# Optimization experiments

Hardware: AMD Instinct MI355X
Metric: run time of the kernel (lower is better)

The kernel has to match this reference:

```python
import jax, jax.numpy as jnp
import numpy as np

EPS = 1e-5
GRID_SIZE = 5
SPLINE_ORDER = 3
WINDOW = 16  # local_window_size hardcoded in Block


def _make_grid(in_features):
    h = 2.0 / GRID_SIZE  # grid_range [-1, 1]
    g = (np.arange(-SPLINE_ORDER, GRID_SIZE + SPLINE_ORDER + 1) * h - 1.0).astype(np.float32)
    return jnp.asarray(np.tile(g[None, :], (in_features, 1)))  # (in, 12)


def layer_norm(x, g, b):
    mu = jnp.mean(x, axis=-1, keepdims=True)
    var = jnp.var(x, axis=-1, keepdims=True)
    return (x - mu) * jax.lax.rsqrt(var + EPS) * g + b


def b_splines(x, grid):
    # x: (M, in) -> (M, in, GRID_SIZE + SPLINE_ORDER)
    xe = x[..., None]
    bases = ((xe >= grid[:, :-1]) & (xe < grid[:, 1:])).astype(x.dtype)
    for k in range(1, SPLINE_ORDER + 1):
        bases = ((xe - grid[:, : -(k + 1)]) / (grid[:, k:-1] - grid[:, : -(k + 1)]) * bases[..., :-1]
                 + (grid[:, k + 1:] - xe) / (grid[:, k + 1:] - grid[:, 1:-k]) * bases[..., 1:])
    return bases


def kan_linear(x, base_w, spline_w, spline_scaler, grid):
    base = jax.nn.silu(x) @ base_w.T  # (M, out)
    sw = spline_w * spline_scaler[..., None]  # (out, in, K)
    spline = jnp.einsum('mik,oik->mo', b_splines(x, grid), sw)
    return base + spline


def conv1d(h, w, b):
    # h: (B, C, T), w: (O, I, 3) or (O, I, k); padding 'same' for k=3 pad=1
    pad = (w.shape[-1] - 1) // 2
    out = jax.lax.conv_general_dilated(h, w, window_strides=(1,), padding=[(pad, pad)],
                                       dimension_numbers=('NCH', 'OIH', 'NCH'))
    return out + b[None, :, None]


def setup_inputs() -> dict:
    key = jax.random.key(0)
    ks = jax.random.split(key, 20)
    B, N, C = 8, 1024, 48
    H = 8
    hid = 24
    K = GRID_SIZE + SPLINE_ORDER
    s = 0.05
    inp = {
        'x': jax.random.normal(ks[0], (B, N, C), dtype=jnp.float32),
        'g1': jnp.ones((C,), jnp.float32), 'b1': jnp.zeros((C,), jnp.float32),
        'w_qkv': jax.random.normal(ks[1], (3 * C, C), jnp.float32) * s,
        'w_proj': jax.random.normal(ks[2], (C, C), jnp.float32) * s,
        'b_proj': jnp.zeros((C,), jnp.float32),
        'g2': jnp.ones((C,), jnp.float32), 'b2': jnp.zeros((C,), jnp.float32),
        'bw1': jax.random.normal(ks[3], (hid, C), jnp.float32) * s,
        'sw1': jax.random.normal(ks[4], (hid, C, K), jnp.float32) * s,
        'ss1': jnp.ones((hid, C), jnp.float32),
        'bw2': jax.random.normal(ks[5], (C, hid), jnp.float32) * s,
        'sw2': jax.random.normal(ks[6], (C, hid, K), jnp.float32) * s,
        'ss2': jnp.ones((C, hid), jnp.float32),
        'conv1_w': jax.random.normal(ks[7], (128, C, 3), jnp.float32) * s,
        'conv1_b': jnp.zeros((128,), jnp.float32),
        'conv3_w': jax.random.normal(ks[8], (C, 128, 3), jnp.float32) * s,
        'conv3_b': jnp.zeros((C,), jnp.float32),
        'sc': jnp.asarray(0.1, jnp.float32),
    }
    return inp


def reference(x, g1, b1, w_qkv, w_proj, b_proj, g2, b2,
              bw1, sw1, ss1, bw2, sw2, ss2,
              conv1_w, conv1_b, conv3_w, conv3_b, sc):
    B, N, C = x.shape
    H = 8
    hd = C // H
    scale = hd ** -0.5

    n1 = layer_norm(x, g1, b1)
    qkv = (n1 @ w_qkv.T).reshape(B, N, 3, H, hd)
    q, k, v = (qkv[:, :, 0].transpose(0, 2, 1, 3),
               qkv[:, :, 1].transpose(0, 2, 1, 3),
               qkv[:, :, 2].transpose(0, 2, 1, 3))  # (B, H, N, hd)

    # global attention
    attn_global = jax.nn.softmax(jnp.einsum('bhqd,bhkd->bhqk', q, k) * scale, axis=-1)
    x_global = jnp.einsum('bhqk,bhkd->bhqd', attn_global, v)
    x_global = x_global.transpose(0, 2, 1, 3).reshape(B, N, C)

    # local (non-overlapping window) attention, vectorized over windows
    W = WINDOW
    nw = N // W
    qw = q.reshape(B, H, nw, W, hd)
    kw = k.reshape(B, H, nw, W, hd)
    vw = v.reshape(B, H, nw, W, hd)
    attn_local = jax.nn.softmax(jnp.einsum('bhnqd,bhnkd->bhnqk', qw, kw) * scale, axis=-1)
    x_local = jnp.einsum('bhnqk,bhnkd->bhnqd', attn_local, vw)
    x_local = x_local.reshape(B, H, N, hd).transpose(0, 2, 1, 3).reshape(B, N, C)

    attn_out = (x_global + x_local) @ w_proj.T + b_proj
    x1 = x + attn_out

    # KAN MLP on norm2(x1), flattened tokens
    n2 = layer_norm(x1, g2, b2).reshape(-1, C)
    grid1 = _make_grid(C)
    grid2 = _make_grid(bw1.shape[0])
    kan_h = kan_linear(n2, bw1, sw1, ss1, grid1)
    kan_o = kan_linear(kan_h, bw2, sw2, ss2, grid2).reshape(B, N, C)
    x2 = x1 + kan_o

    # conv residual path on the original input
    h = x.transpose(0, 2, 1)  # (B, C, N)
    h = conv1d(h, conv1_w, conv1_b)
    h = conv1d(h, conv3_w, conv3_b)
    h = h.transpose(0, 2, 1)  # (B, N, C)
    h = layer_norm(h, g1, b1)  # Block reuses norm1 here

    out = sc * h + x2
    return (out, attn_global)
```

## Files before the change

### kernel.cpp

```cpp
#include <hip/hip_runtime.h>

static constexpr int B = 8, N = 1024, C = 48, H = 8, HD = 6, NT = B * N;
static constexpr int QKVO = 3 * C;
static constexpr int HID = 24, KB = 8;
static constexpr int C1 = 128;

#define DEVFN __device__ __forceinline__

DEVFN float wsum(float v) {
#pragma unroll
  for (int m = 32; m; m >>= 1) v += __shfl_xor(v, m, 64);
  return v;
}
DEVFN float wmax(float v) {
#pragma unroll
  for (int m = 32; m; m >>= 1) v = fmaxf(v, __shfl_xor(v, m, 64));
  return v;
}
DEVFN float gsum16(float v) {
#pragma unroll
  for (int m = 8; m; m >>= 1) v += __shfl_xor(v, m, 16);
  return v;
}
DEVFN float gmax16(float v) {
#pragma unroll
  for (int m = 8; m; m >>= 1) v = fmaxf(v, __shfl_xor(v, m, 16));
  return v;
}

DEVFN void bspline8(float x, float* bs) {
  float b[11];
#pragma unroll
  for (int j = 0; j < 11; ++j) {
    float gj = -2.2f + 0.4f * j;
    float gj1 = -2.2f + 0.4f * (j + 1);
    b[j] = (x >= gj && x < gj1) ? 1.0f : 0.0f;
  }
#pragma unroll
  for (int j = 0; j < 10; ++j) {
    float gj = -2.2f + 0.4f * j;
    b[j] = (x - gj) * 2.5f * b[j] + ((gj + 0.8f) - x) * 2.5f * b[j + 1];
  }
#pragma unroll
  for (int j = 0; j < 9; ++j) {
    float gj = -2.2f + 0.4f * j;
    b[j] = (x - gj) * 1.25f * b[j] + ((gj + 1.2f) - x) * 1.25f * b[j + 1];
  }
#pragma unroll
  for (int j = 0; j < 8; ++j) {
    float gj = -2.2f + 0.4f * j;
    bs[j] = (x - gj) * (1.0f / 1.2f) * b[j] + ((gj + 1.6f) - x) * (1.0f / 1.2f) * b[j + 1];
  }
}

__global__ __launch_bounds__(256) void k_ln_qkv(
    const float* __restrict__ x, const float* __restrict__ g1, const float* __restrict__ b1,
    const float* __restrict__ wqkv, float* __restrict__ q, float* __restrict__ k,
    float* __restrict__ v) {
  __shared__ float wl[QKVO * 49];
  __shared__ float nb[4][C];
  int tid = threadIdx.x;
  for (int e = tid; e < QKVO * C; e += 256) wl[(e / C) * 49 + (e % C)] = wqkv[e];
  int wave = tid >> 6, lane = tid & 63;
  int tok = blockIdx.x * 4 + wave;
  const float* xr = x + tok * C;
  float xv = (lane < C) ? xr[lane] : 0.f;
  float s = wsum(xv), s2 = wsum(xv * xv);
  float mean = s * (1.f / C);
  float var = s2 * (1.f / C) - mean * mean;
  float rstd = rsqrtf(var + 1e-5f);
  if (lane < C) nb[wave][lane] = (xv - mean) * rstd * g1[lane] + b1[lane];
  __syncthreads();
  int b = tok >> 10, n = tok & 1023;
#pragma unroll
  for (int r = 0; r < 3; ++r) {
    int o = lane + (r << 6);
    if (o < QKVO) {
      float acc = 0.f;
#pragma unroll
      for (int i = 0; i < C; ++i) acc += nb[wave][i] * wl[o * 49 + i];
      int ssel = o / C;
      int rem = o - ssel * C;
      int hh = rem / HD;
      int d = rem - hh * HD;
      float* dst = ssel == 0 ? q : (ssel == 1 ? k : v);
      dst[((b * H + hh) * N + n) * HD + d] = acc;
    }
  }
}

__global__ __launch_bounds__(256) void k_gattn(
    const float* __restrict__ q, const float* __restrict__ k, const float* __restrict__ v,
    float* __restrict__ attn, float* __restrict__ xg) {
  __shared__ float2 kt[3][N];
  __shared__ float2 vt[3][N];
  int tid = threadIdx.x;
  int bh = blockIdx.x >> 5;
  int rb = blockIdx.x & 31;
  const float* kg = k + bh * N * HD;
  const float* vg = v + bh * N * HD;
  float* ktf = (float*)kt;
  float* vtf = (float*)vt;
  for (int e = tid; e < N * HD; e += 256) {
    int kp = e / 6, d = e - kp * 6;
    int a = (d >> 1) * 2048 + (kp << 1) + (d & 1);
    ktf[a] = kg[e];
    vtf[a] = vg[e];
  }
  __syncthreads();
  int wave = tid >> 6, lane = tid & 63;
  const float scl = 0.40824829046386301637f;
  int b = bh >> 3, hh = bh & 7;
#pragma unroll 1
  for (int rr = 0; rr < 8; ++rr) {
    int qrow = (rb << 5) + (wave << 3) + rr;
    const float2* qp = (const float2*)(q + (bh * N + qrow) * HD);
    float2 q0 = qp[0], q1 = qp[1], q2 = qp[2];
    float sv[16];
    float mx = -1e30f;
#pragma unroll
    for (int it = 0; it < 16; ++it) {
      int kp = lane + (it << 6);
      float2 a0 = kt[0][kp], a1 = kt[1][kp], a2 = kt[2][kp];
      float dp = q0.x * a0.x + q0.y * a0.y + q1.x * a1.x + q1.y * a1.y + q2.x * a2.x + q2.y * a2.y;
      sv[it] = dp * scl;
      mx = fmaxf(mx, sv[it]);
    }
    mx = wmax(mx);
    float sum = 0.f;
#pragma unroll
    for (int it = 0; it < 16; ++it) {
      sv[it] = __expf(sv[it] - mx);
      sum += sv[it];
    }
    sum = wsum(sum);
    float inv = 1.f / sum;
    float a0 = 0, a1 = 0, a2 = 0, a3 = 0, a4 = 0, a5 = 0;
    float* arow = attn + (size_t)(bh * N + qrow) * N;
#pragma unroll
    for (int it = 0; it < 16; ++it) {
      int kp = lane + (it << 6);
      float p = sv[it];
      arow[kp] = p * inv;
      float2 v0 = vt[0][kp], v1 = vt[1][kp], v2 = vt[2][kp];
      a0 += p * v0.x; a1 += p * v0.y; a2 += p * v1.x;
      a3 += p * v1.y; a4 += p * v2.x; a5 += p * v2.y;
    }
    a0 = wsum(a0) * inv; a1 = wsum(a1) * inv; a2 = wsum(a2) * inv;
    a3 = wsum(a3) * inv; a4 = wsum(a4) * inv; a5 = wsum(a5) * inv;
    if (lane == 0) {
      float* o = xg + (b * N + qrow) * C + hh * HD;
      o[0] = a0; o[1] = a1; o[2] = a2; o[3] = a3; o[4] = a4; o[5] = a5;
    }
  }
}

__global__ __launch_bounds__(256) void k_lattn(
    const float* __restrict__ q, const float* __restrict__ k, const float* __restrict__ v,
    float* __restrict__ xl) {
  int tid = threadIdx.x;
  int wave = tid >> 6, lane = tid & 63;
  int win = blockIdx.x * 4 + wave;
  int bh = win >> 6;
  int wloc = win & 63;
  int n0 = wloc << 4;
  int b = bh >> 3, hh = bh & 7;
  int kk = lane & 15, g = lane >> 4;
  const float* kb = k + (bh * N + n0) * HD;
  const float* vb = v + (bh * N + n0) * HD;
  float kv[6], vv[6];
#pragma unroll
  for (int d = 0; d < 6; ++d) {
    kv[d] = kb[kk * 6 + d];
    vv[d] = vb[kk * 6 + d];
  }
  const float scl = 0.40824829046386301637f;
#pragma unroll
  for (int pass = 0; pass < 4; ++pass) {
    int qr = (pass << 2) + g;
    const float* qp = q + (bh * N + n0 + qr) * HD;
    float s = 0.f;
#pragma unroll
    for (int d = 0; d < 6; ++d) s += qp[d] * kv[d];
    s *= scl;
    float mx = gmax16(s);
    float p = __expf(s - mx);
    float sum = gsum16(p);
    float inv = 1.f / sum;
    float o[6];
#pragma unroll
    for (int d = 0; d < 6; ++d) o[d] = gsum16(p * vv[d]) * inv;
    if (kk == 0) {
      float* dst = xl + (size_t)(b * N + n0 + qr) * C + hh * HD;
#pragma unroll
      for (int d = 0; d < 6; ++d) dst[d] = o[d];
    }
  }
}

__global__ __launch_bounds__(256) void k_proj(
    const float* __restrict__ x, const float* __restrict__ xg, const float* __restrict__ xl,
    const float* __restrict__ wp, const float* __restrict__ bp,
    const float* __restrict__ g2, const float* __restrict__ b2,
    float* __restrict__ x1, float* __restrict__ n2) {
  __shared__ float wl[C * 49];
  __shared__ float ab[4][C];
  int tid = threadIdx.x;
  for (int e = tid; e < C * C; e += 256) wl[(e / C) * 49 + (e % C)] = wp[e];
  int wave = tid >> 6, lane = tid & 63;
  int tok = blockIdx.x * 4 + wave;
  if (lane < C) ab[wave][lane] = xg[tok * C + lane] + xl[tok * C + lane];
  __syncthreads();
  float x1v = 0.f;
  if (lane < C) {
    float acc = bp[lane];
#pragma unroll
    for (int i = 0; i < C; ++i) acc += ab[wave][i] * wl[lane * 49 + i];
    x1v = x[tok * C + lane] + acc;
  }
  float s = wsum(lane < C ? x1v : 0.f);
  float s2 = wsum(lane < C ? x1v * x1v : 0.f);
  float mean = s * (1.f / C), var = s2 * (1.f / C) - mean * mean;
  float rstd = rsqrtf(var + 1e-5f);
  if (lane < C) {
    x1[tok * C + lane] = x1v;
    n2[tok * C + lane] = (x1v - mean) * rstd * g2[lane] + b2[lane];
  }
}

__global__ __launch_bounds__(256) void k_kan1(
    const float* __restrict__ n2, const float* __restrict__ bw1,
    const float* __restrict__ sw1, const float* __restrict__ ss1,
    float* __restrict__ kanh) {
  __shared__ float swt[C * KB * HID];
  __shared__ float bwt[C * HID];
  __shared__ float sst[C * HID];
  __shared__ float bas[4][C][KB];
  __shared__ float sil[4][C];
  int tid = threadIdx.x;
  for (int e = tid; e < C * KB * HID; e += 256) {
    int o = e / (C * KB);
    int rem = e - o * (C * KB);
    swt[rem * HID + o] = sw1[e];
  }
  for (int e = tid; e < C * HID; e += 256) {
    int o = e / C, i = e - o * C;
    bwt[i * HID + o] = bw1[e];
    sst[i * HID + o] = ss1[e];
  }
  int wave = tid >> 6, lane = tid & 63;
  int tok = blockIdx.x * 4 + wave;
  if (lane < C) {
    float xv = n2[tok * C + lane];
    sil[wave][lane] = xv / (1.f + __expf(-xv));
    float bs[KB];
    bspline8(xv, bs);
#pragma unroll
    for (int kk = 0; kk < KB; ++kk) bas[wave][lane][kk] = bs[kk];
  }
  __syncthreads();
  int o = lane & 31;
  int hf = lane >> 5;
  float acc = 0.f;
  if (o < HID) {
    int i0 = hf * 24;
#pragma unroll
    for (int ii = 0; ii < 24; ++ii) {
      int i = i0 + ii;
      float sp = 0.f;
#pragma unroll
      for (int kk = 0; kk < KB; ++kk) sp += bas[wave][i][kk] * swt[(i * KB + kk) * HID + o];
      acc += sil[wave][i] * bwt[i * HID + o] + sst[i * HID + o] * sp;
    }
  }
  acc += __shfl_xor(acc, 32, 64);
  if (lane < HID) kanh[tok * HID + lane] = acc;
}

__global__ __launch_bounds__(256) void k_kan2(
    const float* __restrict__ kanh, const float* __restrict__ x1,
    const float* __restrict__ bw2, const float* __restrict__ sw2,
    const float* __restrict__ ss2, float* __restrict__ x2) {
  __shared__ float swt[HID * KB * C];
  __shared__ float bwt[HID * C];
  __shared__ float sst[HID * C];
  __shared__ float bas[4][HID][KB];
  __shared__ float sil[4][HID];
  int tid = threadIdx.x;
  for (int e = tid; e < HID * KB * C; e += 256) {
    int o = e / (HID * KB);
    int rem = e - o * (HID * KB);
    swt[rem * C + o] = sw2[e];
  }
  for (int e = tid; e < HID * C; e += 256) {
    int o = e / HID, i = e - o * HID;
    bwt[i * C + o] = bw2[e];
    sst[i * C + o] = ss2[e];
  }
  int wave = tid >> 6, lane = tid & 63;
  int tok = blockIdx.x * 4 + wave;
  if (lane < HID) {
    float xv = kanh[tok * HID + lane];
    sil[wave][lane] = xv / (1.f + __expf(-xv));
    float bs[KB];
    bspline8(xv, bs);
#pragma unroll
    for (int kk = 0; kk < KB; ++kk) bas[wave][lane][kk] = bs[kk];
  }
  __syncthreads();
  if (lane < C) {
    float acc = 0.f;
#pragma unroll
    for (int i = 0; i < HID; ++i) {
      float sp = 0.f;
#pragma unroll
      for (int kk = 0; kk < KB; ++kk) sp += bas[wave][i][kk] * swt[(i * KB + kk) * C + lane];
      acc += sil[wave][i] * bwt[i * C + lane] + sst[i * C + lane] * sp;
    }
    x2[tok * C + lane] = x1[tok * C + lane] + acc;
  }
}

__global__ __launch_bounds__(256) void k_conv1(
    const float* __restrict__ x, const float* __restrict__ w1, const float* __restrict__ bc1,
    float* __restrict__ h1) {
  __shared__ float wt[72 * C1];
  __shared__ float xr[18 * C];
  int tid = threadIdx.x;
  int b = blockIdx.x >> 6;
  int t0 = (blockIdx.x & 63) << 4;
  for (int e = tid; e < 18 * C; e += 256) {
    int r = e / C, c = e - r * C;
    int n = t0 - 1 + r;
    xr[e] = (n >= 0 && n < N) ? x[(b * N + n) * C + c] : 0.f;
  }
  int wave = tid >> 6, lane = tid & 63;
  float acc0[4] = {0, 0, 0, 0}, acc1[4] = {0, 0, 0, 0};
  for (int hf = 0; hf < 2; ++hf) {
    __syncthreads();
    for (int e = tid; e < 72 * C1; e += 256) {
      int i3 = e / C1, o = e - i3 * C1;
      int ii = i3 / 3, dk = i3 - ii * 3;
      wt[e] = w1[(o * C + hf * 24 + ii) * 3 + dk];
    }
    __syncthreads();
#pragma unroll
    for (int tt = 0; tt < 4; ++tt) {
      int t = (wave << 2) + tt;
      float a0 = acc0[tt], a1 = acc1[tt];
#pragma unroll 8
      for (int ii = 0; ii < 24; ++ii) {
#pragma unroll
        for (int dk = 0; dk < 3; ++dk) {
          float xin = xr[(t + dk) * C + hf * 24 + ii];
          a0 += xin * wt[(ii * 3 + dk) * C1 + lane];
          a1 += xin * wt[(ii * 3 + dk) * C1 + 64 + lane];
        }
      }
      acc0[tt] = a0;
      acc1[tt] = a1;
    }
  }
  float bb0 = bc1[lane], bb1 = bc1[64 + lane];
#pragma unroll
  for (int tt = 0; tt < 4; ++tt) {
    int n = t0 + (wave << 2) + tt;
    h1[(b * N + n) * C1 + lane] = acc0[tt] + bb0;
    h1[(b * N + n) * C1 + 64 + lane] = acc1[tt] + bb1;
  }
}

__global__ __launch_bounds__(256) void k_conv2out(
    const float* __restrict__ h1, const float* __restrict__ w3, const float* __restrict__ bc3,
    const float* __restrict__ g1, const float* __restrict__ b1,
    const float* __restrict__ x2, const float* __restrict__ scp,
    float* __restrict__ out) {
  __shared__ float wt[192 * C];
  __shared__ float hr[18 * C1];
  int tid = threadIdx.x;
  int b = blockIdx.x >> 6;
  int t0 = (blockIdx.x & 63) << 4;
  for (int e = tid; e < 18 * C1; e += 256) {
    int r = e / C1, c = e - r * C1;
    int n = t0 - 1 + r;
    hr[e] = (n >= 0 && n < N) ? h1[(b * N + n) * C1 + c] : 0.f;
  }
  int wave = tid >> 6, lane = tid & 63;
  float acc[4] = {0, 0, 0, 0};
  for (int hf = 0; hf < 2; ++hf) {
    __syncthreads();
    for (int e = tid; e < 192 * C; e += 256) {
      int i3 = e / C, c = e - i3 * C;
      int ii = i3 / 3, dk = i3 - ii * 3;
      wt[e] = w3[(c * C1 + hf * 64 + ii) * 3 + dk];
    }
    __syncthreads();
    if (lane < C) {
#pragma unroll
      for (int tt = 0; tt < 4; ++tt) {
        int t = (wave << 2) + tt;
        float a = acc[tt];
#pragma unroll 8
        for (int ii = 0; ii < 64; ++ii) {
#pragma unroll
          for (int dk = 0; dk < 3; ++dk) {
            a += hr[(t + dk) * C1 + hf * 64 + ii] * wt[(ii * 3 + dk) * C + lane];
          }
        }
        acc[tt] = a;
      }
    }
  }
  float sc0 = scp[0];
#pragma unroll
  for (int tt = 0; tt < 4; ++tt) {
    int n = t0 + (wave << 2) + tt;
    float val = (lane < C) ? acc[tt] + bc3[lane] : 0.f;
    float s = wsum(val), s2 = wsum(val * val);
    float mean = s * (1.f / C), var = s2 * (1.f / C) - mean * mean;
    float rstd = rsqrtf(var + 1e-5f);
    if (lane < C) {
      float hn = (val - mean) * rstd * g1[lane] + b1[lane];
      out[(b * N + n) * C + lane] = sc0 * hn + x2[(b * N + n) * C + lane];
    }
  }
}

extern "C" void kernel_launch(void* const* d_in, const int* in_sizes, int n_in,
                              void* d_out, int out_size, void* d_ws, size_t ws_size,
                              hipStream_t stream) {
  (void)in_sizes; (void)n_in; (void)out_size; (void)ws_size;
  const float* x    = (const float*)d_in[0];
  const float* g1   = (const float*)d_in[1];
  const float* b1   = (const float*)d_in[2];
  const float* wqkv = (const float*)d_in[3];
  const float* wp   = (const float*)d_in[4];
  const float* bp   = (const float*)d_in[5];
  const float* g2   = (const float*)d_in[6];
  const float* b2   = (const float*)d_in[7];
  const float* bw1  = (const float*)d_in[8];
  const float* sw1  = (const float*)d_in[9];
  const float* ss1  = (const float*)d_in[10];
  const float* bw2  = (const float*)d_in[11];
  const float* sw2  = (const float*)d_in[12];
  const float* ss2  = (const float*)d_in[13];
  const float* w1   = (const float*)d_in[14];
  const float* bc1  = (const float*)d_in[15];
  const float* w3   = (const float*)d_in[16];
  const float* bc3  = (const float*)d_in[17];
  const float* scp  = (const float*)d_in[18];

  float* out  = (float*)d_out;
  float* attn = out + (size_t)NT * C;

  float* ws   = (float*)d_ws;
  float* q    = ws;
  float* k    = ws + 393216;
  float* v    = ws + 786432;
  float* xg   = ws + 1179648;
  float* xl   = ws + 1572864;
  float* x1   = ws + 1966080;
  float* n2   = ws + 2359296;
  float* kanh = ws + 2752512;
  float* x2   = ws;
  float* h1   = ws + 393216;

  k_ln_qkv<<<NT / 4, 256, 0, stream>>>(x, g1, b1, wqkv, q, k, v);
  k_gattn<<<B * H * 32, 256, 0, stream>>>(q, k, v, attn, xg);
  k_lattn<<<B * H * 64 / 4, 256, 0, stream>>>(q, k, v, xl);
  k_proj<<<NT / 4, 256, 0, stream>>>(x, xg, xl, wp, bp, g2, b2, x1, n2);
  k_kan1<<<NT / 4, 256, 0, stream>>>(n2, bw1, sw1, ss1, kanh);
  k_kan2<<<NT / 4, 256, 0, stream>>>(kanh, x1, bw2, sw2, ss2, x2);
  k_conv1<<<512, 256, 0, stream>>>(x, w1, bc1, h1);
  k_conv2out<<<512, 256, 0, stream>>>(h1, w3, bc3, g1, b1, x2, scp, out);
}
```

Before: 552.0 us.

## Fuse local attention into global attention and merge proj/KAN kernels

The local windowed attention now runs inside the global attention kernel, reusing the K/V rows already staged in shared memory. Its result is summed with the global output before a single store. The projection, LayerNorm and both KAN layers are merged into one 512-thread kernel that handles two tokens per wave, removing the intermediate x1/n2/kanh round-trips through global memory and several launches. The attention-matrix writes become nontemporal, and both conv kernels are register-blocked so each loaded input value is reused across four output positions. The trade-offs are fewer, larger attention blocks and a large shared-memory footprint in the fused MLP kernel, which may limit occupancy.

After: 504.0 us. -8.7%, faster.

```diff
diff --git a/kernel.cpp b/kernel.cpp
--- a/kernel.cpp
+++ b/kernel.cpp
@@ -91,12 +91,13 @@
 
 __global__ __launch_bounds__(256) void k_gattn(
     const float* __restrict__ q, const float* __restrict__ k, const float* __restrict__ v,
-    float* __restrict__ attn, float* __restrict__ xg) {
+    float* __restrict__ attn, float* __restrict__ xgl) {
   __shared__ float2 kt[3][N];
   __shared__ float2 vt[3][N];
+  __shared__ float ob[64][6];
   int tid = threadIdx.x;
-  int bh = blockIdx.x >> 5;
-  int rb = blockIdx.x & 31;
+  int bh = blockIdx.x >> 4;
+  int rb = blockIdx.x & 15;
   const float* kg = k + bh * N * HD;
   const float* vg = v + bh * N * HD;
   float* ktf = (float*)kt;
@@ -111,9 +112,10 @@
   int wave = tid >> 6, lane = tid & 63;
   const float scl = 0.40824829046386301637f;
   int b = bh >> 3, hh = bh & 7;
-#pragma unroll 1
-  for (int rr = 0; rr < 8; ++rr) {
-    int qrow = (rb << 5) + (wave << 3) + rr;
+  int r0 = rb * 64 + wave * 16;
+#pragma unroll 2
+  for (int rr = 0; rr < 16; ++rr) {
+    int qrow = r0 + rr;
     const float2* qp = (const float2*)(q + (bh * N + qrow) * HD);
     float2 q0 = qp[0], q1 = qp[1], q2 = qp[2];
     float sv[16];
@@ -141,7 +143,7 @@
     for (int it = 0; it < 16; ++it) {
       int kp = lane + (it << 6);
       float p = sv[it];
-      arow[kp] = p * inv;
+      __builtin_nontemporal_store(p * inv, arow + kp);
       float2 v0 = vt[0][kp], v1 = vt[1][kp], v2 = vt[2][kp];
       a0 += p * v0.x; a1 += p * v0.y; a2 += p * v1.x;
       a3 += p * v1.y; a4 += p * v2.x; a5 += p * v2.y;
@@ -149,36 +151,24 @@
     a0 = wsum(a0) * inv; a1 = wsum(a1) * inv; a2 = wsum(a2) * inv;
     a3 = wsum(a3) * inv; a4 = wsum(a4) * inv; a5 = wsum(a5) * inv;
     if (lane == 0) {
-      float* o = xg + (b * N + qrow) * C + hh * HD;
-      o[0] = a0; o[1] = a1; o[2] = a2; o[3] = a3; o[4] = a4; o[5] = a5;
-    }
-  }
-}
-
-__global__ __launch_bounds__(256) void k_lattn(
-    const float* __restrict__ q, const float* __restrict__ k, const float* __restrict__ v,
-    float* __restrict__ xl) {
-  int tid = threadIdx.x;
-  int wave = tid >> 6, lane = tid & 63;
-  int win = blockIdx.x * 4 + wave;
-  int bh = win >> 6;
-  int wloc = win & 63;
-  int n0 = wloc << 4;
-  int b = bh >> 3, hh = bh & 7;
+      int li = wave * 16 + rr;
+      ob[li][0] = a0; ob[li][1] = a1; ob[li][2] = a2;
+      ob[li][3] = a3; ob[li][4] = a4; ob[li][5] = a5;
+    }
+  }
+  int n0 = r0;
   int kk = lane & 15, g = lane >> 4;
-  const float* kb = k + (bh * N + n0) * HD;
-  const float* vb = v + (bh * N + n0) * HD;
   float kv[6], vv[6];
 #pragma unroll
   for (int d = 0; d < 6; ++d) {
-    kv[d] = kb[kk * 6 + d];
-    vv[d] = vb[kk * 6 + d];
-  }
-  const float scl = 0.40824829046386301637f;
+    int a = (d >> 1) * 2048 + ((n0 + kk) << 1) + (d & 1);
+    kv[d] = ktf[a];
+    vv[d] = vtf[a];
+  }
 #pragma unroll
   for (int pass = 0; pass < 4; ++pass) {
-    int qr = (pass << 2) + g;
-    const float* qp = q + (bh * N + n0 + qr) * HD;
+    int qr = n0 + pass * 4 + g;
+    const float* qp = q + (bh * N + qr) * HD;
     float s = 0.f;
 #pragma unroll
     for (int d = 0; d < 6; ++d) s += qp[d] * kv[d];
@@ -191,133 +181,132 @@
 #pragma unroll
     for (int d = 0; d < 6; ++d) o[d] = gsum16(p * vv[d]) * inv;
     if (kk == 0) {
-      float* dst = xl + (size_t)(b * N + n0 + qr) * C + hh * HD;
-#pragma unroll
-      for (int d = 0; d < 6; ++d) dst[d] = o[d];
-    }
-  }
-}
-
-__global__ __launch_bounds__(256) void k_proj(
-    const float* __restrict__ x, const float* __restrict__ xg, const float* __restrict__ xl,
+      int li = wave * 16 + pass * 4 + g;
+      float* dst = xgl + (size_t)(b * N + qr) * C + hh * HD;
+#pragma unroll
+      for (int d = 0; d < 6; ++d) dst[d] = ob[li][d] + o[d];
+    }
+  }
+}
+
+__global__ __launch_bounds__(512) void k_mlp(
+    const float* __restrict__ x, const float* __restrict__ xgl,
     const float* __restrict__ wp, const float* __restrict__ bp,
     const float* __restrict__ g2, const float* __restrict__ b2,
-    float* __restrict__ x1, float* __restrict__ n2) {
-  __shared__ float wl[C * 49];
-  __shared__ float ab[4][C];
+    const float* __restrict__ bw1, const float* __restrict__ sw1, const float* __restrict__ ss1,
+    const float* __restrict__ bw2, const float* __restrict__ sw2, const float* __restrict__ ss2,
+    float* __restrict__ x2) {
+  __shared__ float wpl[C * 49];
+  __shared__ float bw1t[C * 25];
+  __shared__ float ss1t[C * 25];
+  __shared__ float sw1t[C * KB * 25];
+  __shared__ float bw2t[HID * 49];
+  __shared__ float ss2t[HID * 49];
+  __shared__ float sw2t[HID * KB * 49];
+  __shared__ float abuf[8][2][C];
+  __shared__ float sil1[8][2][C];
+  __shared__ float bas1[8][2][C][KB];
+  __shared__ float sil2[8][2][HID];
+  __shared__ float bas2[8][2][HID][KB];
   int tid = threadIdx.x;
-  for (int e = tid; e < C * C; e += 256) wl[(e / C) * 49 + (e % C)] = wp[e];
+  for (int e = tid; e < C * C; e += 512) wpl[(e / C) * 49 + (e % C)] = wp[e];
+  for (int e = tid; e < HID * C; e += 512) {
+    int o = e / C, i = e - o * C;
+    bw1t[i * 25 + o] = bw1[e];
+    ss1t[i * 25 + o] = ss1[e];
+  }
+  for (int e = tid; e < HID * C * KB; e += 512) {
+    int o = e / (C * KB), r = e - o * (C * KB);
+    sw1t[r * 25 + o] = sw1[e];
+  }
+  for (int e = tid; e < C * HID; e += 512) {
+    int o = e / HID, i = e - o * HID;
+    bw2t[i * 49 + o] = bw2[e];
+    ss2t[i * 49 + o] = ss2[e];
+  }
+  for (int e = tid; e < C * HID * KB; e += 512) {
+    int o = e / (HID * KB), r = e - o * (HID * KB);
+    sw2t[r * 49 + o] = sw2[e];
+  }
+  __syncthreads();
   int wave = tid >> 6, lane = tid & 63;
-  int tok = blockIdx.x * 4 + wave;
-  if (lane < C) ab[wave][lane] = xg[tok * C + lane] + xl[tok * C + lane];
-  __syncthreads();
-  float x1v = 0.f;
+  int tok0 = blockIdx.x * 16 + wave * 2;
+  float x1v[2];
+#pragma unroll
+  for (int tt = 0; tt < 2; ++tt) {
+    int tok = tok0 + tt;
+    float acc = 0.f, xin = 0.f;
+    if (lane < C) {
+      abuf[wave][tt][lane] = xgl[tok * C + lane];
+      xin = x[tok * C + lane];
+    }
+    if (lane < C) {
+      acc = bp[lane];
+#pragma unroll
+      for (int i = 0; i < C; ++i) acc += abuf[wave][tt][i] * wpl[lane * 49 + i];
+    }
+    float xv = (lane < C) ? xin + acc : 0.f;
+    x1v[tt] = xv;
+    float s = wsum(xv), s2 = wsum(xv * xv);
+    float mean = s * (1.f / C), var = s2 * (1.f / C) - mean * mean;
+    float rstd = rsqrtf(var + 1e-5f);
+    if (lane < C) {
+      float n2v = (xv - mean) * rstd * g2[lane] + b2[lane];
+      sil1[wave][tt][lane] = n2v / (1.f + __expf(-n2v));
+      float bs[KB];
+      bspline8(n2v, bs);
+#pragma unroll
+      for (int kk = 0; kk < KB; ++kk) bas1[wave][tt][lane][kk] = bs[kk];
+    }
+  }
+  int o = lane & 31, hf = lane >> 5;
+  float h0 = 0.f, h1 = 0.f;
+  if (o < HID) {
+#pragma unroll 4
+    for (int ii = 0; ii < 24; ++ii) {
+      int i = hf * 24 + ii;
+      float bwv = bw1t[i * 25 + o], ssv = ss1t[i * 25 + o];
+      float sp0 = 0.f, sp1 = 0.f;
+#pragma unroll
+      for (int kk = 0; kk < KB; ++kk) {
+        float w = sw1t[(i * KB + kk) * 25 + o];
+        sp0 += bas1[wave][0][i][kk] * w;
+        sp1 += bas1[wave][1][i][kk] * w;
+      }
+      h0 += sil1[wave][0][i] * bwv + ssv * sp0;
+      h1 += sil1[wave][1][i] * bwv + ssv * sp1;
+    }
+  }
+  h0 += __shfl_xor(h0, 32, 64);
+  h1 += __shfl_xor(h1, 32, 64);
+  if (lane < HID) {
+    float hv[2] = {h0, h1};
+#pragma unroll
+    for (int tt = 0; tt < 2; ++tt) {
+      sil2[wave][tt][lane] = hv[tt] / (1.f + __expf(-hv[tt]));
+      float bs[KB];
+      bspline8(hv[tt], bs);
+#pragma unroll
+      for (int kk = 0; kk < KB; ++kk) bas2[wave][tt][lane][kk] = bs[kk];
+    }
+  }
   if (lane < C) {
-    float acc = bp[lane];
-#pragma unroll
-    for (int i = 0; i < C; ++i) acc += ab[wave][i] * wl[lane * 49 + i];
-    x1v = x[tok * C + lane] + acc;
-  }
-  float s = wsum(lane < C ? x1v : 0.f);
-  float s2 = wsum(lane < C ? x1v * x1v : 0.f);
-  float mean = s * (1.f / C), var = s2 * (1.f / C) - mean * mean;
-  float rstd = rsqrtf(var + 1e-5f);
-  if (lane < C) {
-    x1[tok * C + lane] = x1v;
-    n2[tok * C + lane] = (x1v - mean) * rstd * g2[lane] + b2[lane];
-  }
-}
-
-__global__ __launch_bounds__(256) void k_kan1(
-    const float* __restrict__ n2, const float* __restrict__ bw1,
-    const float* __restrict__ sw1, const float* __restrict__ ss1,
-    float* __restrict__ kanh) {
-  __shared__ float swt[C * KB * HID];
-  __shared__ float bwt[C * HID];
-  __shared__ float sst[C * HID];
-  __shared__ float bas[4][C][KB];
-  __shared__ float sil[4][C];
-  int tid = threadIdx.x;
-  for (int e = tid; e < C * KB * HID; e += 256) {
-    int o = e / (C * KB);
-    int rem = e - o * (C * KB);
-    swt[rem * HID + o] = sw1[e];
-  }
-  for (int e = tid; e < C * HID; e += 256) {
-    int o = e / C, i = e - o * C;
-    bwt[i * HID + o] = bw1[e];
-    sst[i * HID + o] = ss1[e];
-  }
-  int wave = tid >> 6, lane = tid & 63;
-  int tok = blockIdx.x * 4 + wave;
-  if (lane < C) {
-    float xv = n2[tok * C + lane];
-    sil[wave][lane] = xv / (1.f + __expf(-xv));
-    float bs[KB];
-    bspline8(xv, bs);
-#pragma unroll
-    for (int kk = 0; kk < KB; ++kk) bas[wave][lane][kk] = bs[kk];
-  }
-  __syncthreads();
-  int o = lane & 31;
-  int hf = lane >> 5;
-  float acc = 0.f;
-  if (o < HID) {
-    int i0 = hf * 24;
-#pragma unroll
-    for (int ii = 0; ii < 24; ++ii) {
-      int i = i0 + ii;
-      float sp = 0.f;
-#pragma unroll
-      for (int kk = 0; kk < KB; ++kk) sp += bas[wave][i][kk] * swt[(i * KB + kk) * HID + o];
-      acc += sil[wave][i] * bwt[i * HID + o] + sst[i * HID + o] * sp;
-    }
-  }
-  acc += __shfl_xor(acc, 32, 64);
-  if (lane < HID) kanh[tok * HID + lane] = acc;
-}
-
-__global__ __launch_bounds__(256) void k_kan2(
-    const float* __restrict__ kanh, const float* __restrict__ x1,
-    const float* __restrict__ bw2, const float* __restrict__ sw2,
-    const float* __restrict__ ss2, float* __restrict__ x2) {
-  __shared__ float swt[HID * KB * C];
-  __shared__ float bwt[HID * C];
-  __shared__ float sst[HID * C];
-  __shared__ float bas[4][HID][KB];
-  __shared__ float sil[4][HID];
-  int tid = threadIdx.x;
-  for (int e = tid; e < HID * KB * C; e += 256) {
-    int o = e / (HID * KB);
-    int rem = e - o * (HID * KB);
-    swt[rem * C + o] = sw2[e];
-  }
-  for (int e = tid; e < HID * C; e += 256) {
-    int o = e / HID, i = e - o * HID;
-    bwt[i * C + o] = bw2[e];
-    sst[i * C + o] = ss2[e];
-  }
-  int wave = tid >> 6, lane = tid & 63;
-  int tok = blockIdx.x * 4 + wave;
-  if (lane < HID) {
-    float xv = kanh[tok * HID + lane];
-    sil[wave][lane] = xv / (1.f + __expf(-xv));
-    float bs[KB];
-    bspline8(xv, bs);
-#pragma unroll
-    for (int kk = 0; kk < KB; ++kk) bas[wave][lane][kk] = bs[kk];
-  }
-  __syncthreads();
-  if (lane < C) {
-    float acc = 0.f;
-#pragma unroll
+    float a0 = 0.f, a1 = 0.f;
+#pragma unroll 4
     for (int i = 0; i < HID; ++i) {
-      float sp = 0.f;
-#pragma unroll
-      for (int kk = 0; kk < KB; ++kk) sp += bas[wave][i][kk] * swt[(i * KB + kk) * C + lane];
-      acc += sil[wave][i] * bwt[i * C + lane] + sst[i * C + lane] * sp;
-    }
-    x2[tok * C + lane] = x1[tok * C + lane] + acc;
+      float bwv = bw2t[i * 49 + lane], ssv = ss2t[i * 49 + lane];
+      float sp0 = 0.f, sp1 = 0.f;
+#pragma unroll
+      for (int kk = 0; kk < KB; ++kk) {
+        float w = sw2t[(i * KB + kk) * 49 + lane];
+        sp0 += bas2[wave][0][i][kk] * w;
+        sp1 += bas2[wave][1][i][kk] * w;
+      }
+      a0 += sil2[wave][0][i] * bwv + ssv * sp0;
+      a1 += sil2[wave][1][i] * bwv + ssv * sp1;
+    }
+    x2[(size_t)tok0 * C + lane] = x1v[0] + a0;
+    x2[(size_t)(tok0 + 1) * C + lane] = x1v[1] + a1;
   }
 }
 
@@ -335,36 +324,38 @@
     xr[e] = (n >= 0 && n < N) ? x[(b * N + n) * C + c] : 0.f;
   }
   int wave = tid >> 6, lane = tid & 63;
+  int tb = wave << 2;
   float acc0[4] = {0, 0, 0, 0}, acc1[4] = {0, 0, 0, 0};
   for (int hf = 0; hf < 2; ++hf) {
     __syncthreads();
     for (int e = tid; e < 72 * C1; e += 256) {
-      int i3 = e / C1, o = e - i3 * C1;
+      int i3 = e >> 7, o = e & 127;
       int ii = i3 / 3, dk = i3 - ii * 3;
       wt[e] = w1[(o * C + hf * 24 + ii) * 3 + dk];
     }
     __syncthreads();
-#pragma unroll
-    for (int tt = 0; tt < 4; ++tt) {
-      int t = (wave << 2) + tt;
-      float a0 = acc0[tt], a1 = acc1[tt];
-#pragma unroll 8
-      for (int ii = 0; ii < 24; ++ii) {
-#pragma unroll
-        for (int dk = 0; dk < 3; ++dk) {
-          float xin = xr[(t + dk) * C + hf * 24 + ii];
-          a0 += xin * wt[(ii * 3 + dk) * C1 + lane];
-          a1 += xin * wt[(ii * 3 + dk) * C1 + 64 + lane];
+#pragma unroll 4
+    for (int ii = 0; ii < 24; ++ii) {
+      float xv[6];
+#pragma unroll
+      for (int j = 0; j < 6; ++j) xv[j] = xr[(tb + j) * C + hf * 24 + ii];
+#pragma unroll
+      for (int dk = 0; dk < 3; ++dk) {
+        float w0 = wt[(ii * 3 + dk) * C1 + lane];
+        float w1v = wt[(ii * 3 + dk) * C1 + 64 + lane];
+#pragma unroll
+        for (int tt = 0; tt < 4; ++tt) {
+          float xi = xv[tt + dk];
+          acc0[tt] += xi * w0;
+          acc1[tt] += xi * w1v;
         }
       }
-      acc0[tt] = a0;
-      acc1[tt] = a1;
     }
   }
   float bb0 = bc1[lane], bb1 = bc1[64 + lane];
 #pragma unroll
   for (int tt = 0; tt < 4; ++tt) {
-    int n = t0 + (wave << 2) + tt;
+    int n = t0 + tb + tt;
     h1[(b * N + n) * C1 + lane] = acc0[tt] + bb0;
     h1[(b * N + n) * C1 + 64 + lane] = acc1[tt] + bb1;
   }
@@ -375,17 +366,18 @@
     const float* __restrict__ g1, const float* __restrict__ b1,
     const float* __restrict__ x2, const float* __restrict__ scp,
     float* __restrict__ out) {
-  __shared__ float wt[192 * C];
+  __shared__ float wt[192 * C + 16];
   __shared__ float hr[18 * C1];
   int tid = threadIdx.x;
   int b = blockIdx.x >> 6;
   int t0 = (blockIdx.x & 63) << 4;
   for (int e = tid; e < 18 * C1; e += 256) {
-    int r = e / C1, c = e - r * C1;
+    int r = e >> 7, c = e & 127;
     int n = t0 - 1 + r;
     hr[e] = (n >= 0 && n < N) ? h1[(b * N + n) * C1 + c] : 0.f;
   }
   int wave = tid >> 6, lane = tid & 63;
+  int tb = wave << 2;
   float acc[4] = {0, 0, 0, 0};
   for (int hf = 0; hf < 2; ++hf) {
     __syncthreads();
@@ -395,33 +387,30 @@
       wt[e] = w3[(c * C1 + hf * 64 + ii) * 3 + dk];
     }
     __syncthreads();
-    if (lane < C) {
-#pragma unroll
-      for (int tt = 0; tt < 4; ++tt) {
-        int t = (wave << 2) + tt;
-        float a = acc[tt];
-#pragma unroll 8
-        for (int ii = 0; ii < 64; ++ii) {
-#pragma unroll
-          for (int dk = 0; dk < 3; ++dk) {
-            a += hr[(t + dk) * C1 + hf * 64 + ii] * wt[(ii * 3 + dk) * C + lane];
-          }
-        }
-        acc[tt] = a;
+#pragma unroll 4
+    for (int ii = 0; ii < 64; ++ii) {
+      float xv[6];
+#pragma unroll
+      for (int j = 0; j < 6; ++j) xv[j] = hr[(tb + j) * C1 + hf * 64 + ii];
+#pragma unroll
+      for (int dk = 0; dk < 3; ++dk) {
+        float w = wt[(ii * 3 + dk) * C + lane];
+#pragma unroll
+        for (int tt = 0; tt < 4; ++tt) acc[tt] += xv[tt + dk] * w;
       }
     }
   }
   float sc0 = scp[0];
 #pragma unroll
   for (int tt = 0; tt < 4; ++tt) {
-    int n = t0 + (wave << 2) + tt;
+    int n = t0 + tb + tt;
     float val = (lane < C) ? acc[tt] + bc3[lane] : 0.f;
     float s = wsum(val), s2 = wsum(val * val);
     float mean = s * (1.f / C), var = s2 * (1.f / C) - mean * mean;
     float rstd = rsqrtf(var + 1e-5f);
     if (lane < C) {
       float hn = (val - mean) * rstd * g1[lane] + b1[lane];
-      out[(b * N + n) * C + lane] = sc0 * hn + x2[(b * N + n) * C + lane];
+      out[(b * N + n) * C + lane] = sc0 * hn + x2[(size_t)(b * N + n) * C + lane];
     }
   }
 }
@@ -457,20 +446,14 @@
   float* q    = ws;
   float* k    = ws + 393216;
   float* v    = ws + 786432;
-  float* xg   = ws + 1179648;
-  float* xl   = ws + 1572864;
-  float* x1   = ws + 1966080;
-  float* n2   = ws + 2359296;
-  float* kanh = ws + 2752512;
-  float* x2   = ws;
-  float* h1   = ws + 393216;
+  float* xgl  = ws + 1179648;
+  float* x2   = ws + 1572864;
+  float* h1   = ws + 1966080;
 
   k_ln_qkv<<<NT / 4, 256, 0, stream>>>(x, g1, b1, wqkv, q, k, v);
-  k_gattn<<<B * H * 32, 256, 0, stream>>>(q, k, v, attn, xg);
-  k_lattn<<<B * H * 64 / 4, 256, 0, stream>>>(q, k, v, xl);
-  k_proj<<<NT / 4, 256, 0, stream>>>(x, xg, xl, wp, bp, g2, b2, x1, n2);
-  k_kan1<<<NT / 4, 256, 0, stream>>>(n2, bw1, sw1, ss1, kanh);
-  k_kan2<<<NT / 4, 256, 0, stream>>>(kanh, x1, bw2, sw2, ss2, x2);
+  k_gattn<<<B * H * 16, 256, 0, stream>>>(q, k, v, attn, xgl);
+  k_mlp<<<NT / 16, 512, 0, stream>>>(x, xgl, wp, bp, g2, b2,
+                                     bw1, sw1, ss1, bw2, sw2, ss2, x2);
   k_conv1<<<512, 256, 0, stream>>>(x, w1, bc1, h1);
   k_conv2out<<<512, 256, 0, stream>>>(h1, w3, bc3, g1, b1, x2, scp, out);
 }
```
